# Optimization experiments

Measured on AMD Instinct MI355X. Metric: run time of the kernel, lower is better.

The kernel has to match this reference:

```python
import jax, jax.numpy as jnp
import numpy as np

LN_EPS = 1e-5   # torch LayerNorm default
NRM_EPS = 1e-8  # normalizer-state epsilon in mLSTMCell


def setup_inputs() -> dict:
    key = jax.random.key(0)
    ks = jax.random.split(key, 3)
    B, T, H, L, O = 32, 256, 1024, 4, 256
    x = jax.random.normal(ks[0], (B, T, H), dtype=jnp.float32)
    # 6 projections per layer in order (q, k, v, i, f, o); Linear stored as [in, out]
    W = jax.random.normal(ks[1], (L, 6, H, H), dtype=jnp.float32) * 0.02
    b = jnp.zeros((L, 6, H), dtype=jnp.float32)
    ln_g = jnp.ones((L, 6, H), dtype=jnp.float32)
    ln_b = jnp.zeros((L, 6, H), dtype=jnp.float32)
    fc_w = jax.random.normal(ks[2], (H, O), dtype=jnp.float32) * 0.02
    fc_b = jnp.zeros((O,), dtype=jnp.float32)
    return {"x": x, "W": W, "b": b, "ln_g": ln_g, "ln_b": ln_b,
            "fc_w": fc_w, "fc_b": fc_b}


def _layer_norm(z, g, beta):
    # z: [6, B, H]; g, beta: [6, H]
    mu = z.mean(-1, keepdims=True)
    var = z.var(-1, keepdims=True)
    return (z - mu) * jax.lax.rsqrt(var + LN_EPS) * g[:, None, :] + beta[:, None, :]


def _cell(x_in, h_prev, c_prev, n_prev, Wl, bl, gl, betal):
    # x_in: [B, H]; states: [B, H]; Wl: [6, H, H]
    z = jnp.einsum('bh,jhd->jbd', x_in, Wl) + bl[:, None, :]
    z = _layer_norm(z, gl, betal)
    q, k, v, zi, zf, zo = z  # q is computed by the original cell but unused
    i = jnp.exp(zi)
    f = jax.nn.sigmoid(zf)
    o = jax.nn.sigmoid(zo)
    # kv_interaction = outer(k, v); sum over dim=1 == sum(k) * v (same math, no [B,H,H])
    kv_sum = k.sum(-1, keepdims=True) * v
    c = f * c_prev + i * kv_sum
    n = f * n_prev + i * k
    n_hat = n / (jnp.linalg.norm(n, axis=-1, keepdims=True) + NRM_EPS)
    h = o * jnp.tanh(c * n_hat)
    return h, c, n


def _mlstm_forward(x, W, b, ln_g, ln_b, fc_w, fc_b):
    B, T, H = x.shape
    L = W.shape[0]
    h0 = jnp.zeros((L, B, H), x.dtype)
    init = (h0, h0, h0)  # (h, c, n)

    def step(carry, x_t):
        h, c, n = carry
        layer_in = x_t
        hs, cs, ns = [], [], []
        for l in range(L):  # small fixed layer count
            h_l, c_l, n_l = _cell(layer_in, h[l], c[l], n[l],
                                  W[l], b[l], ln_g[l], ln_b[l])
            if l > 0:  # residual connection (use_residual=True)
                h_l = h_l + layer_in
            layer_in = h_l
            hs.append(h_l); cs.append(c_l); ns.append(n_l)
        return (jnp.stack(hs), jnp.stack(cs), jnp.stack(ns)), None

    (h, c, n), _ = jax.lax.scan(step, init, jnp.swapaxes(x, 0, 1))
    # output[-1] == top-layer hidden at the final timestep
    out = h[-1] @ fc_w + fc_b  # [B, O]
    return out, (h, c, n)


def reference(x, W, b, ln_g, ln_b, fc_w, fc_b):
    return _mlstm_forward(x, W, b, ln_g, ln_b, fc_w, fc_b)
```

## Files before the change

### kernel.cpp

```cpp
#include <hip/hip_runtime.h>
#include <hip/hip_bf16.h>
#include <math.h>

#define H 1024
#define B 32
#define T 256
#define L 4
#define O 256
#define SEGLEN 16
#define NSEG (T / SEGLEN)

typedef _Float16 half8 __attribute__((ext_vector_type(8)));
typedef _Float16 half4 __attribute__((ext_vector_type(4)));
typedef float f32x4 __attribute__((ext_vector_type(4)));

#define X_PK_OFF   0
#define HB0_OFF    8388608
#define HB1_OFF    16777216
#define WT2_OFF    25165824
#define Z16_OFF    46137344
#define SEGA_OFF   88080384
#define SEGBC_OFF  89128960
#define SEGBN_OFF  90177536
#define STATS_OFF  91226112
#define CARC_OFF   91422720
#define CARN_OFF   92471296
#define FCP_OFF    93519872

__global__ __launch_bounds__(256) void pack_w(const float* __restrict__ W,
                                              _Float16* __restrict__ Wt2) {
  int tile = blockIdx.x;
  int m_idx = tile >> 8;
  int kt = (tile >> 4) & 15, ntt = tile & 15;
  int l = m_idx / 5, jj = m_idx % 5;
  const float* Wf = W + ((size_t)(l * 6 + jj + 1) << 20);
  _Float16* out = Wt2 + ((size_t)m_idx << 20);
  __shared__ float ts[64][65];
  int k0 = kt * 64, n0 = ntt * 64;
#pragma unroll
  for (int s = 0; s < 16; ++s) {
    int e = threadIdx.x + s * 256;
    int kk = e >> 6, col = e & 63;
    ts[kk][col] = Wf[(size_t)(k0 + kk) * H + n0 + col];
  }
  __syncthreads();
#pragma unroll
  for (int gi = 0; gi < 2; ++gi) {
    int g = threadIdx.x * 2 + gi;
    int l64 = g & 63, ksl = (g >> 6) & 1, ntl = g >> 7;
    int nn = l64 & 15, kh = l64 >> 4;
    half8 tmp;
#pragma unroll
    for (int e = 0; e < 8; ++e)
      tmp[e] = (_Float16)ts[ksl * 32 + kh * 8 + e][ntl * 16 + nn];
    *(half8*)&out[(size_t)((ntt * 4 + ntl) * 32 + kt * 2 + ksl) * 512 + (size_t)l64 * 8] = tmp;
  }
}

__global__ __launch_bounds__(256) void pack_x(const float* __restrict__ x,
                                              _Float16* __restrict__ x_pk) {
  int t = blockIdx.x;
  __shared__ float ld[32][257];
  for (int c = 0; c < 4; ++c) {
#pragma unroll
    for (int s = 0; s < 32; ++s) {
      int e2 = threadIdx.x + s * 256;
      int b = e2 >> 8, col = e2 & 255;
      ld[b][col] = x[((size_t)b * T + t) * H + c * 256 + col];
    }
    __syncthreads();
#pragma unroll
    for (int s3 = 0; s3 < 4; ++s3) {
      int gg = threadIdx.x * 4 + s3;
      int l64 = gg & 63, ksl = (gg >> 6) & 7, bt = gg >> 9;
      int nn = l64 & 15, kh = l64 >> 4;
      int b = bt * 16 + nn;
      half8 tmp;
#pragma unroll
      for (int e = 0; e < 8; ++e)
        tmp[e] = (_Float16)ld[b][ksl * 32 + kh * 8 + e];
      *(half8*)&x_pk[(size_t)t * 32768 + (size_t)bt * 16384 +
                     (size_t)(c * 8 + ksl) * 512 + (size_t)l64 * 8] = tmp;
    }
    __syncthreads();
  }
}

__global__ __launch_bounds__(512) void gemm_big(
    const _Float16* __restrict__ A_pk, const _Float16* __restrict__ Wl,
    _Float16* __restrict__ z16) {
  int raw = blockIdx.x;
  int xcd = raw & 7, c = raw >> 3;
  int bm = (xcd >> 1) * 16 + (c & 15);
  int bn = (xcd & 1) * 10 + (c >> 4);
  int w = threadIdx.x >> 6, lane = threadIdx.x & 63;
  int wm = w >> 2, wn = w & 3;

  __shared__ _Float16 smem[24576];

  int j = bn >> 2;
  const _Float16* gsrc[3];
  int ldst[3];
#pragma unroll
  for (int q = 0; q < 3; ++q) {
    int f = w * 3 + q;
    if (f < 8) {
      gsrc[q] = A_pk + (size_t)(bm * 8 + f) * 16384 + lane * 8;
      ldst[q] = f * 512 + lane * 8;
    } else {
      int nf = f - 8;
      gsrc[q] = Wl + ((size_t)j << 20) + (size_t)((bn & 3) * 16 + nf) * 16384 + lane * 8;
      ldst[q] = 4096 + nf * 512 + lane * 8;
    }
  }

  half8 stA[3], stB[3];
#pragma unroll
  for (int q = 0; q < 3; ++q) stA[q] = *(const half8*)(gsrc[q]);
#pragma unroll
  for (int q = 0; q < 3; ++q) *(half8*)&smem[ldst[q]] = stA[q];
#pragma unroll
  for (int q = 0; q < 3; ++q) stA[q] = *(const half8*)(gsrc[q] + 512);
  __syncthreads();

  f32x4 acc[4][4] = {};
  int ardo = wm * 2048 + lane * 8;
  int brdo = 4096 + wn * 2048 + lane * 8;

  for (int ks = 0; ks < 32; ks += 2) {
    {
      if (ks + 2 < 32) {
#pragma unroll
        for (int q = 0; q < 3; ++q)
          stB[q] = *(const half8*)(gsrc[q] + (size_t)(ks + 2) * 512);
      }
      half8 a[4], b[4];
#pragma unroll
      for (int i = 0; i < 4; ++i) a[i] = *(const half8*)&smem[ardo + i * 512];
#pragma unroll
      for (int i = 0; i < 4; ++i) b[i] = *(const half8*)&smem[brdo + i * 512];
#pragma unroll
      for (int i = 0; i < 4; ++i)
#pragma unroll
        for (int jf = 0; jf < 4; ++jf)
          acc[i][jf] = __builtin_amdgcn_mfma_f32_16x16x32_f16(a[i], b[jf], acc[i][jf], 0, 0, 0);
#pragma unroll
      for (int q = 0; q < 3; ++q) *(half8*)&smem[12288 + ldst[q]] = stA[q];
      asm volatile("s_waitcnt lgkmcnt(0)" ::: "memory");
      __builtin_amdgcn_s_barrier();
      __builtin_amdgcn_sched_barrier(0);
    }
    {
      if (ks + 3 < 32) {
#pragma unroll
        for (int q = 0; q < 3; ++q)
          stA[q] = *(const half8*)(gsrc[q] + (size_t)(ks + 3) * 512);
      }
      half8 a[4], b[4];
#pragma unroll
      for (int i = 0; i < 4; ++i) a[i] = *(const half8*)&smem[12288 + ardo + i * 512];
#pragma unroll
      for (int i = 0; i < 4; ++i) b[i] = *(const half8*)&smem[12288 + brdo + i * 512];
#pragma unroll
      for (int i = 0; i < 4; ++i)
#pragma unroll
        for (int jf = 0; jf < 4; ++jf)
          acc[i][jf] = __builtin_amdgcn_mfma_f32_16x16x32_f16(a[i], b[jf], acc[i][jf], 0, 0, 0);
      if (ks + 2 < 32) {
#pragma unroll
        for (int q = 0; q < 3; ++q) *(half8*)&smem[ldst[q]] = stB[q];
        asm volatile("s_waitcnt lgkmcnt(0)" ::: "memory");
        __builtin_amdgcn_s_barrier();
        __builtin_amdgcn_sched_barrier(0);
      }
    }
  }
  __syncthreads();

  _Float16 (*cz)[264] = (_Float16(*)[264])smem;
  int hb0 = (bn & 3) * 256;
  for (int p = 0; p < 2; ++p) {
    if (p) __syncthreads();
    if (wm == p) {
#pragma unroll
      for (int i = 0; i < 4; ++i)
#pragma unroll
        for (int jf = 0; jf < 4; ++jf)
#pragma unroll
          for (int r = 0; r < 4; ++r)
            cz[i * 16 + (lane >> 4) * 4 + r][wn * 64 + jf * 16 + (lane & 15)] =
                (_Float16)acc[i][jf][r];
    }
    __syncthreads();
#pragma unroll
    for (int s = 0; s < 4; ++s) {
      int e = threadIdx.x + s * 512;
      int r = e >> 5, h8 = e & 31;
      int m_local = bm * 128 + p * 64 + r;
      half8 vv = *(const half8*)&cz[r][h8 * 8];
      *(half8*)&z16[((size_t)m_local * 5 + j) * 1024 + hb0 + h8 * 8] = vv;
    }
  }
}

__global__ __launch_bounds__(256) void stats_kernel(
    const _Float16* __restrict__ z16, const float* __restrict__ bias,
    const float* __restrict__ ln_g, const float* __restrict__ ln_b,
    float* __restrict__ stats, int l) {
  int row = blockIdx.x, tid = threadIdx.x;
  int h0 = tid * 4;
  float red[13];
#pragma unroll
  for (int jj = 0; jj < 5; ++jj) {
    half4 z4 = *(const half4*)&z16[((size_t)row * 5 + jj) * 1024 + h0];
    float4 bb = *(const float4*)&bias[(size_t)(l * 6 + 1 + jj) * H + h0];
    float vx = (float)z4[0] + bb.x, vy = (float)z4[1] + bb.y,
          vz = (float)z4[2] + bb.z, vw = (float)z4[3] + bb.w;
    red[jj * 2] = vx + vy + vz + vw;
    red[jj * 2 + 1] = vx * vx + vy * vy + vz * vz + vw * vw;
    if (jj == 0) {
      float4 g = *(const float4*)&ln_g[(size_t)(l * 6 + 1) * H + h0];
      float4 be = *(const float4*)&ln_b[(size_t)(l * 6 + 1) * H + h0];
      red[10] = vx * g.x + vy * g.y + vz * g.z + vw * g.w;
      red[11] = g.x + g.y + g.z + g.w;
      red[12] = be.x + be.y + be.z + be.w;
    }
  }
#pragma unroll
  for (int off = 32; off; off >>= 1)
#pragma unroll
    for (int q = 0; q < 13; ++q) red[q] += __shfl_down(red[q], off);
  __shared__ float sb[4][13];
  if ((tid & 63) == 0) {
#pragma unroll
    for (int q = 0; q < 13; ++q) sb[tid >> 6][q] = red[q];
  }
  __syncthreads();
  if (tid == 0) {
    float st[13];
#pragma unroll
    for (int q = 0; q < 13; ++q) st[q] = sb[0][q] + sb[1][q] + sb[2][q] + sb[3][q];
    float* so = stats + (size_t)row * 12;
#pragma unroll
    for (int jj = 0; jj < 5; ++jj) {
      float mu = st[jj * 2] * (1.0f / H);
      float var = st[jj * 2 + 1] * (1.0f / H) - mu * mu;
      so[jj * 2] = mu;
      so[jj * 2 + 1] = rsqrtf(var + 1e-5f);
    }
    float mu0 = st[0] * (1.0f / H);
    float rs0 = rsqrtf(st[1] * (1.0f / H) - mu0 * mu0 + 1e-5f);
    so[10] = rs0 * (st[10] - mu0 * st[11]) + st[12];
    so[11] = 0.f;
  }
}

__global__ __launch_bounds__(256) void scan_p1agg(
    const _Float16* __restrict__ z16, const float* __restrict__ stats,
    const float* __restrict__ bias, const float* __restrict__ ln_g,
    const float* __restrict__ ln_b, float* __restrict__ segA,
    float* __restrict__ segBc, float* __restrict__ segBn, int l) {
  int idx = blockIdx.x * 256 + threadIdx.x;
  int h = idx & 1023;
  int bs = idx >> 10;
  int b = bs & 31, seg = bs >> 5;

  float bz[4], gg[4], bb[4];
#pragma unroll
  for (int jj = 0; jj < 4; ++jj) {
    bz[jj] = bias[(size_t)(l * 6 + 1 + jj) * H + h];
    gg[jj] = ln_g[(size_t)(l * 6 + 1 + jj) * H + h];
    bb[jj] = ln_b[(size_t)(l * 6 + 1 + jj) * H + h];
  }
  float A = 1.f, bc = 0.f, bn = 0.f;
#pragma unroll 2
  for (int u = 0; u < SEGLEN; ++u) {
    int row = (seg * SEGLEN + u) * 32 + b;
    size_t zb = ((size_t)row * 5) * 1024 + h;
    float zk = (float)z16[zb];
    float zv = (float)z16[zb + 1024];
    float zi = (float)z16[zb + 2048];
    float zf = (float)z16[zb + 3072];
    const float* st = stats + (size_t)row * 12;
    float k   = (zk + bz[0] - st[0]) * st[1] * gg[0] + bb[0];
    float v   = (zv + bz[1] - st[2]) * st[3] * gg[1] + bb[1];
    float zi_ = (zi + bz[2] - st[4]) * st[5] * gg[2] + bb[2];
    float zf_ = (zf + bz[3] - st[6]) * st[7] * gg[3] + bb[3];
    float iv = __expf(zi_);
    float fv = 1.f / (1.f + __expf(-zf_));
    A *= fv;
    bn = fv * bn + iv * k;
    bc = fv * bc + iv * (st[10] * v);
  }
  size_t so = ((size_t)seg * 32 + b) * 1024 + h;
  segA[so] = A;
  segBn[so] = bn;
  segBc[so] = bc;
}

__global__ __launch_bounds__(256) void scan_p2(
    const float* __restrict__ segA, const float* __restrict__ segBc,
    const float* __restrict__ segBn, float* __restrict__ carC,
    float* __restrict__ carN) {
  int idx = blockIdx.x * 256 + threadIdx.x;
  int h = idx & 1023, b = idx >> 10;
  float cc = 0.f, nn = 0.f;
#pragma unroll
  for (int seg = 0; seg < NSEG; ++seg) {
    size_t coff = (size_t)seg * 32768 + (size_t)b * 1024 + h;
    carC[coff] = cc;
    carN[coff] = nn;
    size_t so = ((size_t)seg * 32 + b) * 1024 + h;
    float a = segA[so];
    cc = segBc[so] + a * cc;
    nn = segBn[so] + a * nn;
  }
}

__global__ __launch_bounds__(256) void final_scan(
    const _Float16* __restrict__ z16, const float* __restrict__ stats,
    const float* __restrict__ bias, const float* __restrict__ ln_g,
    const float* __restrict__ ln_b, const float* __restrict__ carC,
    const float* __restrict__ carN, const _Float16* __restrict__ hin,
    _Float16* __restrict__ hout, float* __restrict__ out, int l) {
  int seg = blockIdx.x >> 5, b = blockIdx.x & 31;
  int tid = threadIdx.x, h0 = tid * 4;

  float bz[5][4], gg[5][4], bb[5][4];
#pragma unroll
  for (int jj = 0; jj < 5; ++jj) {
    float4 t1 = *(const float4*)&bias[(size_t)(l * 6 + 1 + jj) * H + h0];
    float4 t2 = *(const float4*)&ln_g[(size_t)(l * 6 + 1 + jj) * H + h0];
    float4 t3 = *(const float4*)&ln_b[(size_t)(l * 6 + 1 + jj) * H + h0];
    bz[jj][0] = t1.x; bz[jj][1] = t1.y; bz[jj][2] = t1.z; bz[jj][3] = t1.w;
    gg[jj][0] = t2.x; gg[jj][1] = t2.y; gg[jj][2] = t2.z; gg[jj][3] = t2.w;
    bb[jj][0] = t3.x; bb[jj][1] = t3.y; bb[jj][2] = t3.z; bb[jj][3] = t3.w;
  }

  size_t coff = (size_t)seg * 32768 + (size_t)b * 1024 + h0;
  float4 cC4 = *(const float4*)&carC[coff];
  float4 cN4 = *(const float4*)&carN[coff];
  float c_[4] = {cC4.x, cC4.y, cC4.z, cC4.w};
  float n_[4] = {cN4.x, cN4.y, cN4.z, cN4.w};

  size_t hfoff = (size_t)(b >> 4) * 16384 + (size_t)(h0 >> 5) * 512 +
                 (size_t)((((h0 & 31) >> 3) * 16) + (b & 15)) * 8 + (h0 & 7);
  __shared__ float sbuf[2][4];

  half4 zr[5];
  {
    int row0 = (seg * SEGLEN) * 32 + b;
#pragma unroll
    for (int jj = 0; jj < 5; ++jj)
      zr[jj] = *(const half4*)&z16[((size_t)row0 * 5 + jj) * 1024 + h0];
  }

  for (int u = 0; u < SEGLEN; ++u) {
    int t = seg * SEGLEN + u;
    int row = t * 32 + b;
    half4 zc[5];
#pragma unroll
    for (int jj = 0; jj < 5; ++jj) zc[jj] = zr[jj];
    if (u + 1 < SEGLEN) {
      int rown = (t + 1) * 32 + b;
#pragma unroll
      for (int jj = 0; jj < 5; ++jj)
        zr[jj] = *(const half4*)&z16[((size_t)rown * 5 + jj) * 1024 + h0];
    }
    half4 rin;
    if (l > 0) rin = *(const half4*)&hin[(size_t)t * 32768 + hfoff];

    const float* st = stats + (size_t)row * 12;
    float mu0 = st[0], rs0 = st[1], mu1 = st[2], rs1 = st[3];
    float mu2 = st[4], rs2 = st[5], mu3 = st[6], rs3 = st[7];
    float mu4 = st[8], rs4 = st[9], ksum = st[10];

    float ss = 0.f;
#pragma unroll
    for (int e = 0; e < 4; ++e) {
      float k   = ((float)zc[0][e] + bz[0][e] - mu0) * rs0 * gg[0][e] + bb[0][e];
      float v   = ((float)zc[1][e] + bz[1][e] - mu1) * rs1 * gg[1][e] + bb[1][e];
      float zi_ = ((float)zc[2][e] + bz[2][e] - mu2) * rs2 * gg[2][e] + bb[2][e];
      float zf_ = ((float)zc[3][e] + bz[3][e] - mu3) * rs3 * gg[3][e] + bb[3][e];
      float iv = __expf(zi_);
      float fv = 1.f / (1.f + __expf(-zf_));
      n_[e] = fv * n_[e] + iv * k;
      c_[e] = fv * c_[e] + iv * (ksum * v);
      ss += n_[e] * n_[e];
    }
#pragma unroll
    for (int off = 32; off; off >>= 1) ss += __shfl_down(ss, off);
    if ((tid & 63) == 0) sbuf[u & 1][tid >> 6] = ss;
    __syncthreads();
    float nrm = sbuf[u & 1][0] + sbuf[u & 1][1] + sbuf[u & 1][2] + sbuf[u & 1][3];
    float rn = 1.f / (sqrtf(nrm) + 1e-8f);

    float hh[4];
#pragma unroll
    for (int e = 0; e < 4; ++e) {
      float zo_ = ((float)zc[4][e] + bz[4][e] - mu4) * rs4 * gg[4][e] + bb[4][e];
      float ov = 1.f / (1.f + __expf(-zo_));
      float targ = c_[e] * (n_[e] * rn);
      float e2 = __expf(-2.f * fabsf(targ));
      float th = copysignf((1.f - e2) / (1.f + e2), targ);
      hh[e] = ov * th + ((l > 0) ? (float)rin[e] : 0.f);
    }
    half4 hx;
    hx[0] = (_Float16)hh[0]; hx[1] = (_Float16)hh[1];
    hx[2] = (_Float16)hh[2]; hx[3] = (_Float16)hh[3];
    *(half4*)&hout[(size_t)t * 32768 + hfoff] = hx;

    if (t == T - 1) {
      *(float4*)&out[8192 + (size_t)l * 32768 + (size_t)b * 1024 + h0] =
          make_float4(hh[0], hh[1], hh[2], hh[3]);
      *(float4*)&out[8192 + 131072 + ((size_t)(l * B) + b) * 1024 + h0] =
          make_float4(c_[0], c_[1], c_[2], c_[3]);
      *(float4*)&out[8192 + 262144 + ((size_t)(l * B) + b) * 1024 + h0] =
          make_float4(n_[0], n_[1], n_[2], n_[3]);
    }
  }
}

__global__ __launch_bounds__(256) void fc_part(
    const float* __restrict__ out_h, const float* __restrict__ fc_w,
    float* __restrict__ partial) {
  int b = blockIdx.x >> 3, kh = blockIdx.x & 7;
  int o = threadIdx.x;
  const float* hr = out_h + (size_t)b * 1024 + kh * 128;
  const float* wp = fc_w + (size_t)kh * 128 * O + o;
  float acc = 0.f;
#pragma unroll 8
  for (int h = 0; h < 128; ++h)
    acc = fmaf(hr[h], wp[(size_t)h * O], acc);
  partial[((size_t)kh * 32 + b) * O + o] = acc;
}

__global__ __launch_bounds__(256) void fc_reduce(
    const float* __restrict__ partial, const float* __restrict__ fc_b,
    float* __restrict__ out) {
  int b = blockIdx.x, o = threadIdx.x;
  float acc = fc_b[o];
#pragma unroll
  for (int kh = 0; kh < 8; ++kh)
    acc += partial[((size_t)kh * 32 + b) * O + o];
  out[(size_t)b * O + o] = acc;
}

extern "C" void kernel_launch(void* const* d_in, const int* in_sizes, int n_in,
                              void* d_out, int out_size, void* d_ws, size_t ws_size,
                              hipStream_t stream) {
  const float* x    = (const float*)d_in[0];
  const float* W    = (const float*)d_in[1];
  const float* bias = (const float*)d_in[2];
  const float* ln_g = (const float*)d_in[3];
  const float* ln_b = (const float*)d_in[4];
  const float* fc_w = (const float*)d_in[5];
  const float* fc_b = (const float*)d_in[6];
  float* out = (float*)d_out;
  _Float16* wsh = (_Float16*)d_ws;

  _Float16* x_pk = wsh + X_PK_OFF;
  _Float16* hb[2] = {wsh + HB0_OFF, wsh + HB1_OFF};
  _Float16* Wt2  = wsh + WT2_OFF;
  _Float16* z16  = wsh + Z16_OFF;
  float* segA  = (float*)(wsh + SEGA_OFF);
  float* segBc = (float*)(wsh + SEGBC_OFF);
  float* segBn = (float*)(wsh + SEGBN_OFF);
  float* stats = (float*)(wsh + STATS_OFF);
  float* carC  = (float*)(wsh + CARC_OFF);
  float* carN  = (float*)(wsh + CARN_OFF);
  float* fcp   = (float*)(wsh + FCP_OFF);

  pack_w<<<5120, 256, 0, stream>>>(W, Wt2);
  pack_x<<<256, 256, 0, stream>>>(x, x_pk);

  for (int l = 0; l < L; ++l) {
    const _Float16* A_in = (l == 0) ? x_pk : hb[(l - 1) & 1];
    _Float16* h_out = hb[l & 1];
    const _Float16* Wl = Wt2 + ((size_t)(l * 5) << 20);
    gemm_big<<<1280, 512, 0, stream>>>(A_in, Wl, z16);
    stats_kernel<<<8192, 256, 0, stream>>>(z16, bias, ln_g, ln_b, stats, l);
    scan_p1agg<<<2048, 256, 0, stream>>>(z16, stats, bias, ln_g, ln_b,
                                         segA, segBc, segBn, l);
    scan_p2<<<128, 256, 0, stream>>>(segA, segBc, segBn, carC, carN);
    final_scan<<<512, 256, 0, stream>>>(z16, stats, bias, ln_g, ln_b,
                                        carC, carN, A_in, h_out, out, l);
  }
  fc_part<<<256, 256, 0, stream>>>(out + 8192 + 3 * 32768, fc_w, fcp);
  fc_reduce<<<B, 256, 0, stream>>>(fcp, fc_b, out);
}
```

Measured before the change: 753.7 us.

## Fuse LayerNorm row statistics into GEMM epilogue with partial sums

The GEMM epilogue now computes per-row partial sums, sums of squares and the gamma-weighted dot for each 256-column tile it writes. These go to a psum buffer, and a small finalize kernel combines them into the mean and rstd stats. This replaces the separate stats kernel, which re-read the whole z16 tensor from memory every layer. The gamma and beta totals move into a one-time kernel. In exchange the epilogue does extra loads, shuffles and global writes, and the stats are now computed from the fp16-rounded values.

```diff
diff --git a/kernel.cpp b/kernel.cpp
--- a/kernel.cpp
+++ b/kernel.cpp
@@ -26,6 +26,8 @@
 #define CARC_OFF   91422720
 #define CARN_OFF   92471296
 #define FCP_OFF    93519872
+#define PSUM_OFF   93650944
+#define GSUM_OFF   94961664
 
 __global__ __launch_bounds__(256) void pack_w(const float* __restrict__ W,
                                               _Float16* __restrict__ Wt2) {
@@ -86,9 +88,33 @@
   }
 }
 
+__global__ __launch_bounds__(256) void gsum_kernel(
+    const float* __restrict__ ln_g, const float* __restrict__ ln_b,
+    float* __restrict__ gsums) {
+  int l = blockIdx.x;
+  int tid = threadIdx.x;
+  float4 g4 = *(const float4*)&ln_g[(size_t)(l * 6 + 1) * H + tid * 4];
+  float4 b4 = *(const float4*)&ln_b[(size_t)(l * 6 + 1) * H + tid * 4];
+  float sg = g4.x + g4.y + g4.z + g4.w;
+  float sb = b4.x + b4.y + b4.z + b4.w;
+#pragma unroll
+  for (int off = 32; off; off >>= 1) {
+    sg += __shfl_down(sg, off);
+    sb += __shfl_down(sb, off);
+  }
+  __shared__ float sm[8];
+  if ((tid & 63) == 0) { sm[tid >> 6] = sg; sm[(tid >> 6) + 4] = sb; }
+  __syncthreads();
+  if (tid == 0) {
+    gsums[l * 2]     = sm[0] + sm[1] + sm[2] + sm[3];
+    gsums[l * 2 + 1] = sm[4] + sm[5] + sm[6] + sm[7];
+  }
+}
+
 __global__ __launch_bounds__(512) void gemm_big(
     const _Float16* __restrict__ A_pk, const _Float16* __restrict__ Wl,
-    _Float16* __restrict__ z16) {
+    const float* __restrict__ bias, const float* __restrict__ ln_g,
+    _Float16* __restrict__ z16, float* __restrict__ psum, int l) {
   int raw = blockIdx.x;
   int xcd = raw & 7, c = raw >> 3;
   int bm = (xcd >> 1) * 16 + (c & 15);
@@ -193,66 +219,63 @@
     }
     __syncthreads();
 #pragma unroll
-    for (int s = 0; s < 4; ++s) {
-      int e = threadIdx.x + s * 512;
+    for (int sph = 0; sph < 4; ++sph) {
+      int e = threadIdx.x + sph * 512;
       int r = e >> 5, h8 = e & 31;
       int m_local = bm * 128 + p * 64 + r;
       half8 vv = *(const half8*)&cz[r][h8 * 8];
       *(half8*)&z16[((size_t)m_local * 5 + j) * 1024 + hb0 + h8 * 8] = vv;
-    }
-  }
-}
-
-__global__ __launch_bounds__(256) void stats_kernel(
-    const _Float16* __restrict__ z16, const float* __restrict__ bias,
-    const float* __restrict__ ln_g, const float* __restrict__ ln_b,
+      const float* bp = bias + (size_t)(l * 6 + 1 + j) * H + hb0 + h8 * 8;
+      const float* gp = ln_g + (size_t)(l * 6 + 1) * H + hb0 + h8 * 8;
+      float s = 0.f, sq = 0.f, sk = 0.f;
+#pragma unroll
+      for (int q2 = 0; q2 < 8; ++q2) {
+        float val = (float)vv[q2] + bp[q2];
+        s += val;
+        sq += val * val;
+        if (j == 0) sk += val * gp[q2];
+      }
+#pragma unroll
+      for (int off = 16; off; off >>= 1) {
+        s  += __shfl_xor(s, off, 32);
+        sq += __shfl_xor(sq, off, 32);
+        if (j == 0) sk += __shfl_xor(sk, off, 32);
+      }
+      if ((threadIdx.x & 31) == 0)
+        *(float4*)&psum[((size_t)bn * 8192 + m_local) * 4] =
+            make_float4(s, sq, sk, 0.f);
+    }
+  }
+}
+
+__global__ __launch_bounds__(256) void stats_finalize(
+    const float* __restrict__ psum, const float* __restrict__ gsums,
     float* __restrict__ stats, int l) {
-  int row = blockIdx.x, tid = threadIdx.x;
-  int h0 = tid * 4;
-  float red[13];
+  int row = blockIdx.x * 256 + threadIdx.x;
+  float* so = stats + (size_t)row * 12;
+  float mu0 = 0.f, rs0 = 0.f;
 #pragma unroll
   for (int jj = 0; jj < 5; ++jj) {
-    half4 z4 = *(const half4*)&z16[((size_t)row * 5 + jj) * 1024 + h0];
-    float4 bb = *(const float4*)&bias[(size_t)(l * 6 + 1 + jj) * H + h0];
-    float vx = (float)z4[0] + bb.x, vy = (float)z4[1] + bb.y,
-          vz = (float)z4[2] + bb.z, vw = (float)z4[3] + bb.w;
-    red[jj * 2] = vx + vy + vz + vw;
-    red[jj * 2 + 1] = vx * vx + vy * vy + vz * vz + vw * vw;
-    if (jj == 0) {
-      float4 g = *(const float4*)&ln_g[(size_t)(l * 6 + 1) * H + h0];
-      float4 be = *(const float4*)&ln_b[(size_t)(l * 6 + 1) * H + h0];
-      red[10] = vx * g.x + vy * g.y + vz * g.z + vw * g.w;
-      red[11] = g.x + g.y + g.z + g.w;
-      red[12] = be.x + be.y + be.z + be.w;
-    }
-  }
-#pragma unroll
-  for (int off = 32; off; off >>= 1)
-#pragma unroll
-    for (int q = 0; q < 13; ++q) red[q] += __shfl_down(red[q], off);
-  __shared__ float sb[4][13];
-  if ((tid & 63) == 0) {
-#pragma unroll
-    for (int q = 0; q < 13; ++q) sb[tid >> 6][q] = red[q];
-  }
-  __syncthreads();
-  if (tid == 0) {
-    float st[13];
-#pragma unroll
-    for (int q = 0; q < 13; ++q) st[q] = sb[0][q] + sb[1][q] + sb[2][q] + sb[3][q];
-    float* so = stats + (size_t)row * 12;
-#pragma unroll
-    for (int jj = 0; jj < 5; ++jj) {
-      float mu = st[jj * 2] * (1.0f / H);
-      float var = st[jj * 2 + 1] * (1.0f / H) - mu * mu;
-      so[jj * 2] = mu;
-      so[jj * 2 + 1] = rsqrtf(var + 1e-5f);
-    }
-    float mu0 = st[0] * (1.0f / H);
-    float rs0 = rsqrtf(st[1] * (1.0f / H) - mu0 * mu0 + 1e-5f);
-    so[10] = rs0 * (st[10] - mu0 * st[11]) + st[12];
-    so[11] = 0.f;
-  }
+    float s = 0.f, sq = 0.f;
+#pragma unroll
+    for (int q = 0; q < 4; ++q) {
+      size_t off = ((size_t)(jj * 4 + q) * 8192 + row) * 4;
+      s += psum[off];
+      sq += psum[off + 1];
+    }
+    float mu = s * (1.0f / H);
+    float var = sq * (1.0f / H) - mu * mu;
+    float rs = rsqrtf(var + 1e-5f);
+    so[jj * 2] = mu;
+    so[jj * 2 + 1] = rs;
+    if (jj == 0) { mu0 = mu; rs0 = rs; }
+  }
+  float sk = 0.f;
+#pragma unroll
+  for (int q = 0; q < 4; ++q)
+    sk += psum[((size_t)q * 8192 + row) * 4 + 2];
+  so[10] = rs0 * (sk - mu0 * gsums[l * 2]) + gsums[l * 2 + 1];
+  so[11] = 0.f;
 }
 
 __global__ __launch_bounds__(256) void scan_p1agg(
@@ -470,16 +493,19 @@
   float* carC  = (float*)(wsh + CARC_OFF);
   float* carN  = (float*)(wsh + CARN_OFF);
   float* fcp   = (float*)(wsh + FCP_OFF);
+  float* psum  = (float*)(wsh + PSUM_OFF);
+  float* gsums = (float*)(wsh + GSUM_OFF);
 
   pack_w<<<5120, 256, 0, stream>>>(W, Wt2);
   pack_x<<<256, 256, 0, stream>>>(x, x_pk);
+  gsum_kernel<<<4, 256, 0, stream>>>(ln_g, ln_b, gsums);
 
   for (int l = 0; l < L; ++l) {
     const _Float16* A_in = (l == 0) ? x_pk : hb[(l - 1) & 1];
     _Float16* h_out = hb[l & 1];
     const _Float16* Wl = Wt2 + ((size_t)(l * 5) << 20);
-    gemm_big<<<1280, 512, 0, stream>>>(A_in, Wl, z16);
-    stats_kernel<<<8192, 256, 0, stream>>>(z16, bias, ln_g, ln_b, stats, l);
+    gemm_big<<<1280, 512, 0, stream>>>(A_in, Wl, bias, ln_g, z16, psum, l);
+    stats_finalize<<<32, 256, 0, stream>>>(psum, gsums, stats, l);
     scan_p1agg<<<2048, 256, 0, stream>>>(z16, stats, bias, ln_g, ln_b,
                                          segA, segBc, segBn, l);
     scan_p2<<<128, 256, 0, stream>>>(segA, segBc, segBn, carC, carN);
```

New measurement: 793.7 us. +5.3%, slower.

## Fuse LayerNorm stats kernel into segment-aggregate scan pass

Applied to the files above, without the earlier changes.

Merges the per-row LayerNorm statistics kernel and the first scan pass into one kernel. Each block owns one (segment, batch) pair and walks its timesteps, computing row statistics with a block reduction and then applying the scan update directly. This drops one launch per layer and a second read of the z16 activations, with next-row loads prefetched. In exchange the grid shrinks to 512 blocks and every timestep now needs two block-wide barriers, which may reduce parallelism and latency hiding.

```diff
diff --git a/kernel.cpp b/kernel.cpp
--- a/kernel.cpp
+++ b/kernel.cpp
@@ -203,99 +203,118 @@
   }
 }
 
-__global__ __launch_bounds__(256) void stats_kernel(
+__global__ __launch_bounds__(256) void scan_p1fused(
     const _Float16* __restrict__ z16, const float* __restrict__ bias,
     const float* __restrict__ ln_g, const float* __restrict__ ln_b,
-    float* __restrict__ stats, int l) {
-  int row = blockIdx.x, tid = threadIdx.x;
-  int h0 = tid * 4;
-  float red[13];
+    float* __restrict__ stats, float* __restrict__ segA,
+    float* __restrict__ segBc, float* __restrict__ segBn, int l) {
+  int seg = blockIdx.x >> 5, b = blockIdx.x & 31;
+  int tid = threadIdx.x, h0 = tid * 4;
+
+  float bz[5][4], gg[5][4], bb[5][4];
 #pragma unroll
   for (int jj = 0; jj < 5; ++jj) {
-    half4 z4 = *(const half4*)&z16[((size_t)row * 5 + jj) * 1024 + h0];
-    float4 bb = *(const float4*)&bias[(size_t)(l * 6 + 1 + jj) * H + h0];
-    float vx = (float)z4[0] + bb.x, vy = (float)z4[1] + bb.y,
-          vz = (float)z4[2] + bb.z, vw = (float)z4[3] + bb.w;
-    red[jj * 2] = vx + vy + vz + vw;
-    red[jj * 2 + 1] = vx * vx + vy * vy + vz * vz + vw * vw;
-    if (jj == 0) {
-      float4 g = *(const float4*)&ln_g[(size_t)(l * 6 + 1) * H + h0];
-      float4 be = *(const float4*)&ln_b[(size_t)(l * 6 + 1) * H + h0];
-      red[10] = vx * g.x + vy * g.y + vz * g.z + vw * g.w;
-      red[11] = g.x + g.y + g.z + g.w;
-      red[12] = be.x + be.y + be.z + be.w;
-    }
-  }
-#pragma unroll
-  for (int off = 32; off; off >>= 1)
-#pragma unroll
-    for (int q = 0; q < 13; ++q) red[q] += __shfl_down(red[q], off);
+    float4 t1 = *(const float4*)&bias[(size_t)(l * 6 + 1 + jj) * H + h0];
+    float4 t2 = *(const float4*)&ln_g[(size_t)(l * 6 + 1 + jj) * H + h0];
+    float4 t3 = *(const float4*)&ln_b[(size_t)(l * 6 + 1 + jj) * H + h0];
+    bz[jj][0] = t1.x; bz[jj][1] = t1.y; bz[jj][2] = t1.z; bz[jj][3] = t1.w;
+    gg[jj][0] = t2.x; gg[jj][1] = t2.y; gg[jj][2] = t2.z; gg[jj][3] = t2.w;
+    bb[jj][0] = t3.x; bb[jj][1] = t3.y; bb[jj][2] = t3.z; bb[jj][3] = t3.w;
+  }
+
+  float A[4] = {1.f, 1.f, 1.f, 1.f};
+  float bc[4] = {0.f, 0.f, 0.f, 0.f};
+  float bn[4] = {0.f, 0.f, 0.f, 0.f};
   __shared__ float sb[4][13];
-  if ((tid & 63) == 0) {
-#pragma unroll
-    for (int q = 0; q < 13; ++q) sb[tid >> 6][q] = red[q];
-  }
-  __syncthreads();
-  if (tid == 0) {
+
+  half4 zr[5];
+  {
+    int row0 = (seg * SEGLEN) * 32 + b;
+#pragma unroll
+    for (int jj = 0; jj < 5; ++jj)
+      zr[jj] = *(const half4*)&z16[((size_t)row0 * 5 + jj) * 1024 + h0];
+  }
+
+  for (int u = 0; u < SEGLEN; ++u) {
+    int row = (seg * SEGLEN + u) * 32 + b;
+    half4 zc[5];
+#pragma unroll
+    for (int jj = 0; jj < 5; ++jj) zc[jj] = zr[jj];
+    if (u + 1 < SEGLEN) {
+      int rown = (seg * SEGLEN + u + 1) * 32 + b;
+#pragma unroll
+      for (int jj = 0; jj < 5; ++jj)
+        zr[jj] = *(const half4*)&z16[((size_t)rown * 5 + jj) * 1024 + h0];
+    }
+    float v[5][4];
+    float red[13];
+#pragma unroll
+    for (int jj = 0; jj < 5; ++jj) {
+      float s = 0.f, sq = 0.f;
+#pragma unroll
+      for (int e = 0; e < 4; ++e) {
+        float val = (float)zc[jj][e] + bz[jj][e];
+        v[jj][e] = val;
+        s += val;
+        sq += val * val;
+      }
+      red[jj * 2] = s;
+      red[jj * 2 + 1] = sq;
+      if (jj == 0) {
+        red[10] = v[0][0] * gg[0][0] + v[0][1] * gg[0][1] +
+                  v[0][2] * gg[0][2] + v[0][3] * gg[0][3];
+        red[11] = gg[0][0] + gg[0][1] + gg[0][2] + gg[0][3];
+        red[12] = bb[0][0] + bb[0][1] + bb[0][2] + bb[0][3];
+      }
+    }
+#pragma unroll
+    for (int off = 32; off; off >>= 1)
+#pragma unroll
+      for (int q = 0; q < 13; ++q) red[q] += __shfl_xor(red[q], off);
+    if ((tid & 63) == 0) {
+#pragma unroll
+      for (int q = 0; q < 13; ++q) sb[tid >> 6][q] = red[q];
+    }
+    __syncthreads();
     float st[13];
 #pragma unroll
-    for (int q = 0; q < 13; ++q) st[q] = sb[0][q] + sb[1][q] + sb[2][q] + sb[3][q];
-    float* so = stats + (size_t)row * 12;
+    for (int q = 0; q < 13; ++q)
+      st[q] = sb[0][q] + sb[1][q] + sb[2][q] + sb[3][q];
+    __syncthreads();
+
+    float mus[5], rss[5];
 #pragma unroll
     for (int jj = 0; jj < 5; ++jj) {
       float mu = st[jj * 2] * (1.0f / H);
       float var = st[jj * 2 + 1] * (1.0f / H) - mu * mu;
-      so[jj * 2] = mu;
-      so[jj * 2 + 1] = rsqrtf(var + 1e-5f);
-    }
-    float mu0 = st[0] * (1.0f / H);
-    float rs0 = rsqrtf(st[1] * (1.0f / H) - mu0 * mu0 + 1e-5f);
-    so[10] = rs0 * (st[10] - mu0 * st[11]) + st[12];
-    so[11] = 0.f;
-  }
-}
-
-__global__ __launch_bounds__(256) void scan_p1agg(
-    const _Float16* __restrict__ z16, const float* __restrict__ stats,
-    const float* __restrict__ bias, const float* __restrict__ ln_g,
-    const float* __restrict__ ln_b, float* __restrict__ segA,
-    float* __restrict__ segBc, float* __restrict__ segBn, int l) {
-  int idx = blockIdx.x * 256 + threadIdx.x;
-  int h = idx & 1023;
-  int bs = idx >> 10;
-  int b = bs & 31, seg = bs >> 5;
-
-  float bz[4], gg[4], bb[4];
-#pragma unroll
-  for (int jj = 0; jj < 4; ++jj) {
-    bz[jj] = bias[(size_t)(l * 6 + 1 + jj) * H + h];
-    gg[jj] = ln_g[(size_t)(l * 6 + 1 + jj) * H + h];
-    bb[jj] = ln_b[(size_t)(l * 6 + 1 + jj) * H + h];
-  }
-  float A = 1.f, bc = 0.f, bn = 0.f;
-#pragma unroll 2
-  for (int u = 0; u < SEGLEN; ++u) {
-    int row = (seg * SEGLEN + u) * 32 + b;
-    size_t zb = ((size_t)row * 5) * 1024 + h;
-    float zk = (float)z16[zb];
-    float zv = (float)z16[zb + 1024];
-    float zi = (float)z16[zb + 2048];
-    float zf = (float)z16[zb + 3072];
-    const float* st = stats + (size_t)row * 12;
-    float k   = (zk + bz[0] - st[0]) * st[1] * gg[0] + bb[0];
-    float v   = (zv + bz[1] - st[2]) * st[3] * gg[1] + bb[1];
-    float zi_ = (zi + bz[2] - st[4]) * st[5] * gg[2] + bb[2];
-    float zf_ = (zf + bz[3] - st[6]) * st[7] * gg[3] + bb[3];
-    float iv = __expf(zi_);
-    float fv = 1.f / (1.f + __expf(-zf_));
-    A *= fv;
-    bn = fv * bn + iv * k;
-    bc = fv * bc + iv * (st[10] * v);
-  }
-  size_t so = ((size_t)seg * 32 + b) * 1024 + h;
-  segA[so] = A;
-  segBn[so] = bn;
-  segBc[so] = bc;
+      mus[jj] = mu;
+      rss[jj] = rsqrtf(var + 1e-5f);
+    }
+    float ksum = rss[0] * (st[10] - mus[0] * st[11]) + st[12];
+    if (tid < 12) {
+      float val;
+      if (tid < 10) val = (tid & 1) ? rss[tid >> 1] : mus[tid >> 1];
+      else if (tid == 10) val = ksum;
+      else val = 0.f;
+      stats[(size_t)row * 12 + tid] = val;
+    }
+#pragma unroll
+    for (int e = 0; e < 4; ++e) {
+      float k   = (v[0][e] - mus[0]) * rss[0] * gg[0][e] + bb[0][e];
+      float vv  = (v[1][e] - mus[1]) * rss[1] * gg[1][e] + bb[1][e];
+      float zi_ = (v[2][e] - mus[2]) * rss[2] * gg[2][e] + bb[2][e];
+      float zf_ = (v[3][e] - mus[3]) * rss[3] * gg[3][e] + bb[3][e];
+      float iv = __expf(zi_);
+      float fv = 1.f / (1.f + __expf(-zf_));
+      A[e] *= fv;
+      bn[e] = fv * bn[e] + iv * k;
+      bc[e] = fv * bc[e] + iv * (ksum * vv);
+    }
+  }
+  size_t so = ((size_t)seg * 32 + b) * 1024 + h0;
+  *(float4*)&segA[so]  = make_float4(A[0], A[1], A[2], A[3]);
+  *(float4*)&segBn[so] = make_float4(bn[0], bn[1], bn[2], bn[3]);
+  *(float4*)&segBc[so] = make_float4(bc[0], bc[1], bc[2], bc[3]);
 }
 
 __global__ __launch_bounds__(256) void scan_p2(
@@ -479,9 +498,8 @@
     _Float16* h_out = hb[l & 1];
     const _Float16* Wl = Wt2 + ((size_t)(l * 5) << 20);
     gemm_big<<<1280, 512, 0, stream>>>(A_in, Wl, z16);
-    stats_kernel<<<8192, 256, 0, stream>>>(z16, bias, ln_g, ln_b, stats, l);
-    scan_p1agg<<<2048, 256, 0, stream>>>(z16, stats, bias, ln_g, ln_b,
-                                         segA, segBc, segBn, l);
+    scan_p1fused<<<512, 256, 0, stream>>>(z16, bias, ln_g, ln_b, stats,
+                                          segA, segBc, segBn, l);
     scan_p2<<<128, 256, 0, stream>>>(segA, segBc, segBn, carC, carN);
     final_scan<<<512, 256, 0, stream>>>(z16, stats, bias, ln_g, ln_b,
                                         carC, carN, A_in, h_out, out, l);
```

Result: no change. 767.1 us (+1.8%).
